# Kernel optimization log

Measured on AMD Instinct MI355X. Metric: run time of the kernel, lower is better.

Reference implementation:

```python
import jax, jax.numpy as jnp
import numpy as np

B, T, F = 2048, 128, 1
H1, H2 = 128, 64


def lstm_relu(x, W, U, b):
    """Keras LSTM with activation=relu, recurrent_activation=sigmoid.
    x: [B, T, Fin]; W: [Fin, 4H]; U: [H, 4H]; b: [4H]. Gate order i,f,g,o.
    Returns full sequence of hidden states [B, T, H]."""
    Bb = x.shape[0]
    H = U.shape[0]

    def step(carry, xt):
        h, c = carry
        z = xt @ W + h @ U + b  # [B, 4H]
        i, f, g, o = jnp.split(z, 4, axis=-1)
        i = jax.nn.sigmoid(i)
        f = jax.nn.sigmoid(f)
        o = jax.nn.sigmoid(o)
        g = jax.nn.relu(g)
        c = f * c + i * g
        h = o * jax.nn.relu(c)
        return (h, c), h

    h0 = jnp.zeros((Bb, H), x.dtype)
    (_, _), hs = jax.lax.scan(step, (h0, h0), jnp.swapaxes(x, 0, 1))
    return jnp.swapaxes(hs, 0, 1)  # [B, T, H]


def setup_inputs() -> dict:
    key = jax.random.key(0)
    ks = jax.random.split(key, 16)
    s = 0.05  # small init so relu LSTM stays numerically stable
    d = {
        "x": jax.random.normal(ks[0], (B, T, F), jnp.float32),
        "W1": jax.random.normal(ks[1], (F, 4 * H1), jnp.float32) * s,
        "U1": jax.random.normal(ks[2], (H1, 4 * H1), jnp.float32) * s,
        "b1": jnp.zeros((4 * H1,), jnp.float32),
        "W2": jax.random.normal(ks[3], (H1, 4 * H2), jnp.float32) * s,
        "U2": jax.random.normal(ks[4], (H2, 4 * H2), jnp.float32) * s,
        "b2": jnp.zeros((4 * H2,), jnp.float32),
        "W3": jax.random.normal(ks[5], (H2, 4 * H2), jnp.float32) * s,
        "U3": jax.random.normal(ks[6], (H2, 4 * H2), jnp.float32) * s,
        "b3": jnp.zeros((4 * H2,), jnp.float32),
        "W4": jax.random.normal(ks[7], (H2, 4 * H1), jnp.float32) * s,
        "U4": jax.random.normal(ks[8], (H1, 4 * H1), jnp.float32) * s,
        "b4": jnp.zeros((4 * H1,), jnp.float32),
        "Wd": jax.random.normal(ks[9], (H1, 1), jnp.float32) * s,
        "bd": jnp.zeros((1,), jnp.float32),
    }
    return d


def reference(x, W1, U1, b1, W2, U2, b2, W3, U3, b3, W4, U4, b4, Wd, bd):
    h = lstm_relu(x, W1, U1, b1)            # [B, T, 128]
    h = lstm_relu(h, W2, U2, b2)[:, -1]     # return_sequences=False -> [B, 64]
    h = jnp.broadcast_to(h[:, None, :], (h.shape[0], T, h.shape[-1]))  # RepeatVector
    h = lstm_relu(h, W3, U3, b3)            # [B, T, 64]
    h = lstm_relu(h, W4, U4, b4)            # [B, T, 128]
    out = h @ Wd + bd                       # TimeDistributed Dense(1) -> [B, T, 1]
    return out
```

## Files before the change

### kernel.cpp

```cpp
#include <hip/hip_runtime.h>


#define TSEQ 128
#define NTH  512
#define BSTR 408

typedef __attribute__((ext_vector_type(8))) short bf16x8;
typedef __attribute__((ext_vector_type(4))) float f32x4;
typedef __attribute__((ext_vector_type(2))) float f32x2;
typedef __attribute__((ext_vector_type(4))) short s16x4;
typedef unsigned short ushort_t;

#define FB_L1 0
#define FB_L2 256
#define FB_L3 448
#define FB_L4 512
#define FB_W3 896
#define WS_FRAGS 960
#define WS_NEEDED (WS_FRAGS * 1024)

__device__ __forceinline__ ushort_t f2bf(float f) {
    union { float f; unsigned u; } a; a.f = f;
    unsigned r = a.u + 0x7FFF + ((a.u >> 16) & 1);
    return (ushort_t)(r >> 16);
}
__device__ __forceinline__ float bf2f(ushort_t h) {
    union { unsigned u; float f; } a; a.u = ((unsigned)h) << 16;
    return a.f;
}
__device__ __forceinline__ float sigm(float z) { return 1.0f / (1.0f + __expf(-z)); }

__device__ __forceinline__ f32x4 MF(bf16x8 a, bf16x8 b, f32x4 c) {
    return __builtin_amdgcn_mfma_f32_16x16x32_bf16(a, b, c, 0, 0, 0);
}

__device__ __forceinline__ unsigned cvtpk(float lo, float hi) {
    unsigned r;
    asm("v_cvt_pk_bf16_f32 %0, %1, %2" : "=v"(r) : "v"(lo), "v"(hi));
    return r;
}

__global__ void pack_weights(const float* __restrict__ U1, const float* __restrict__ W2,
                             const float* __restrict__ U2, const float* __restrict__ U3,
                             const float* __restrict__ W4, const float* __restrict__ U4,
                             const float* __restrict__ W3, ushort_t* __restrict__ out)
{
    const int f = blockIdx.x;
    const int lane = threadIdx.x;
    int fl, KT, ldm, ksplit = 1 << 30, ld2 = 0;
    const float *base, *base2 = nullptr;
    if (f < 256)      { fl = f;       KT = 4; ldm = 512; base = U1; }
    else if (f < 448) { fl = f - 256; KT = 6; ldm = 256; base = W2; ksplit = 128; base2 = U2; ld2 = 256; }
    else if (f < 512) { fl = f - 448; KT = 2; ldm = 256; base = U3; }
    else if (f < 896) { fl = f - 512; KT = 6; ldm = 512; base = W4; ksplit = 64;  base2 = U4; ld2 = 512; }
    else              { fl = f - 896; KT = 2; ldm = 256; base = W3; }
    const int jt = fl / (KT * 2);
    const int rem = fl % (KT * 2);
    const int kt = rem >> 1;
    const int s = rem & 1;
    const int j = jt * 16 + (lane & 15);
    ushort_t* o = out + f * 512 + lane * 8;
    #pragma unroll
    for (int i = 0; i < 8; ++i) {
        const int k = kt * 32 + (lane >> 4) * 8 + i;
        const float w = (k < ksplit) ? base[k * ldm + j] : base2[(k - ksplit) * ld2 + j];
        const ushort_t hi = f2bf(w);
        o[i] = s ? f2bf(w - bf2f(hi)) : hi;
    }
}

__global__ __launch_bounds__(NTH, 1) void lstm_mfma_kernel(
    const float* __restrict__ x,
    const float* __restrict__ W1, const float* __restrict__ b1,
    const float* __restrict__ b2, const float* __restrict__ b3,
    const float* __restrict__ b4,
    const float* __restrict__ Wd, const float* __restrict__ bd,
    const ushort_t* __restrict__ wsp,
    float* __restrict__ out)
{
    __shared__ __align__(16) ushort_t bU[16][BSTR];
    __shared__ __align__(16) float obuf[16][128];
    __shared__ __align__(16) float xls[16][132];
    __shared__ __align__(16) float w1ls[512], b1ls[512], b4ls[512], b2ls[256];
    __shared__ __align__(16) ushort_t wlds[96 * 512];

    const int tid  = threadIdx.x;
    const int wid  = tid >> 6;
    const int lane = tid & 63;
    const int quad = lane >> 4;
    const int l15  = lane & 15;
    const int r0   = blockIdx.x * 16;
    const bf16x8* A = (const bf16x8*)wsp;

    {
        unsigned* p = (unsigned*)&bU[0][0];
        for (int i = tid; i < 16 * BSTR / 2; i += NTH) p[i] = 0u;
        const int srow = tid >> 5, scol = (tid & 31) * 4;
        *(f32x4*)&xls[srow][scol] = *(const f32x4*)&x[(r0 + srow) * TSEQ + scol];
        w1ls[tid] = W1[tid];
        b1ls[tid] = b1[tid];
        b4ls[tid] = b4[tid];
        if (tid < 256) b2ls[tid] = b2[tid];
        const ushort_t* src = wsp + FB_L2 * 512;
        for (int i = tid; i < 96 * 64; i += NTH) {
            const int f = i >> 6, c = (i & 63) * 8;
            *(bf16x8*)&wlds[f * 512 + c] = *(const bf16x8*)&src[f * 1024 + c];
        }
    }

    const int hcb = 16 * wid + quad * 4;
    const float wd0 = Wd[lane], wd1 = Wd[64 + lane], bd0 = bd[0];

    float c1r[4] = {0.f, 0.f, 0.f, 0.f};
    float c4r[4] = {0.f, 0.f, 0.f, 0.f};

    __syncthreads();

    {
        bf16x8 wL1[16];
        #pragma unroll
        for (int q = 0; q < 4; ++q)
            #pragma unroll
            for (int kt = 0; kt < 4; ++kt)
                wL1[q * 4 + kt] = A[(FB_L1 + ((wid + 8 * q) * 4 + kt) * 2) * 64 + lane];
        float c2r[4] = {0.f, 0.f, 0.f, 0.f};

        for (int t = 0; t < TSEQ; ++t) {
            const int rb1 = (t & 1) * 128, wb1 = 128 - rb1;
            const int h2w = 256 + (t & 1) * 64;
            const int h2r = 256 + (((t & 1) ^ 1)) * 64;

            {
                bf16x8 Bh[4];
                #pragma unroll
                for (int kt = 0; kt < 4; ++kt)
                    Bh[kt] = *(const bf16x8*)&bU[l15][rb1 + kt * 32 + quad * 8];
                const float xr = xls[l15][t];
                f32x4 acc[4];
                #pragma unroll
                for (int q = 0; q < 4; ++q) {
                    const int jb = (wid + 8 * q) * 16 + quad * 4;
                    f32x4 a = *(const f32x4*)&b1ls[jb];
                    a += xr * *(const f32x4*)&w1ls[jb];
                    #pragma unroll
                    for (int kt = 0; kt < 4; ++kt)
                        a = MF(wL1[q * 4 + kt], Bh[kt], a);
                    acc[q] = a;
                }
                float hg[4];
                #pragma unroll
                for (int g = 0; g < 4; ++g) {
                    const float zi = acc[0][g];
                    const float zf = acc[1][g];
                    const float zg = acc[2][g];
                    const float zo = acc[3][g];
                    const float c = sigm(zf) * c1r[g] + sigm(zi) * fmaxf(zg, 0.f);
                    c1r[g] = c;
                    hg[g] = sigm(zo) * fmaxf(c, 0.f);
                }
                uint2 hv;
                hv.x = cvtpk(hg[0], hg[1]);
                hv.y = cvtpk(hg[2], hg[3]);
                *(uint2*)&bU[l15][wb1 + hcb] = hv;
            }
            __syncthreads();

            if (wid < 4) {
                bf16x8 Bh[6];
                #pragma unroll
                for (int kt = 0; kt < 4; ++kt)
                    Bh[kt] = *(const bf16x8*)&bU[l15][wb1 + kt * 32 + quad * 8];
                Bh[4] = *(const bf16x8*)&bU[l15][h2r + quad * 8];
                Bh[5] = *(const bf16x8*)&bU[l15][h2r + 32 + quad * 8];
                f32x4 acc[4];
                #pragma unroll
                for (int g = 0; g < 4; ++g) {
                    f32x4 a = *(const f32x4*)&b2ls[(4 * g + wid) * 16 + quad * 4];
                    #pragma unroll
                    for (int kt = 0; kt < 6; ++kt) {
                        const bf16x8 w = *(const bf16x8*)&wlds[((4 * g + wid) * 6 + kt) * 512 + lane * 8];
                        a = MF(w, Bh[kt], a);
                    }
                    acc[g] = a;
                }
                float hg[4];
                #pragma unroll
                for (int e = 0; e < 4; ++e) {
                    const float zi = acc[0][e];
                    const float zf = acc[1][e];
                    const float zg = acc[2][e];
                    const float zo = acc[3][e];
                    const float c = sigm(zf) * c2r[e] + sigm(zi) * fmaxf(zg, 0.f);
                    c2r[e] = c;
                    hg[e] = sigm(zo) * fmaxf(c, 0.f);
                }
                uint2 hv;
                hv.x = cvtpk(hg[0], hg[1]);
                hv.y = cvtpk(hg[2], hg[3]);
                *(uint2*)&bU[l15][h2w + wid * 16 + quad * 4] = hv;
            }
        }
    }
    __syncthreads();

    f32x4 z3r[4];
    if (wid < 4) {
        const bf16x8 Bh0 = *(const bf16x8*)&bU[l15][320 + quad * 8];
        const bf16x8 Bh1 = *(const bf16x8*)&bU[l15][320 + 32 + quad * 8];
        #pragma unroll
        for (int g = 0; g < 4; ++g) {
            const int jt = 4 * g + wid;
            f32x4 a = *(const f32x4*)&b3[jt * 16 + quad * 4];
            a = MF(A[(FB_W3 + (jt * 2 + 0) * 2) * 64 + lane], Bh0, a);
            a = MF(A[(FB_W3 + (jt * 2 + 1) * 2) * 64 + lane], Bh1, a);
            z3r[g] = a;
        }
    }
    __syncthreads();
    {
        unsigned* p = (unsigned*)&bU[0][0];
        for (int i = tid; i < 16 * BSTR / 2; i += NTH) p[i] = 0u;
        c4r[0] = c4r[1] = c4r[2] = c4r[3] = 0.f;
        const ushort_t* src = wsp + FB_L3 * 512;
        for (int i = tid; i < 32 * 64; i += NTH) {
            const int f = i >> 6, c = (i & 63) * 8;
            *(bf16x8*)&wlds[f * 512 + c] = *(const bf16x8*)&src[f * 1024 + c];
        }
    }
    __syncthreads();

    {
        bf16x8 wL4[24];
        #pragma unroll
        for (int q = 0; q < 4; ++q)
            #pragma unroll
            for (int kt = 0; kt < 6; ++kt)
                wL4[q * 6 + kt] = A[(FB_L4 + ((wid + 8 * q) * 6 + kt) * 2) * 64 + lane];
        float c3r[4] = {0.f, 0.f, 0.f, 0.f};

        for (int t = 0; t < TSEQ; ++t) {
            const int rb3 = (t & 1) * 64, wb3 = 64 - rb3;
            const int rb4 = 128 + (t & 1) * 128;
            const int wb4 = (rb4 == 128) ? 256 : 128;

            if (wid < 4) {
                const bf16x8 Bh0 = *(const bf16x8*)&bU[l15][rb3 + quad * 8];
                const bf16x8 Bh1 = *(const bf16x8*)&bU[l15][rb3 + 32 + quad * 8];
                f32x4 acc[4];
                #pragma unroll
                for (int g = 0; g < 4; ++g) {
                    f32x4 a = z3r[g];
                    const bf16x8 w0 = *(const bf16x8*)&wlds[((4 * g + wid) * 2 + 0) * 512 + lane * 8];
                    const bf16x8 w1 = *(const bf16x8*)&wlds[((4 * g + wid) * 2 + 1) * 512 + lane * 8];
                    a = MF(w0, Bh0, a);
                    a = MF(w1, Bh1, a);
                    acc[g] = a;
                }
                float hg[4];
                #pragma unroll
                for (int e = 0; e < 4; ++e) {
                    const float zi = acc[0][e];
                    const float zf = acc[1][e];
                    const float zg = acc[2][e];
                    const float zo = acc[3][e];
                    const float c = sigm(zf) * c3r[e] + sigm(zi) * fmaxf(zg, 0.f);
                    c3r[e] = c;
                    hg[e] = sigm(zo) * fmaxf(c, 0.f);
                }
                uint2 hv;
                hv.x = cvtpk(hg[0], hg[1]);
                hv.y = cvtpk(hg[2], hg[3]);
                *(uint2*)&bU[l15][wb3 + wid * 16 + quad * 4] = hv;
            }
            __syncthreads();

            {
                bf16x8 Bh[6];
                #pragma unroll
                for (int kt = 0; kt < 2; ++kt)
                    Bh[kt] = *(const bf16x8*)&bU[l15][wb3 + kt * 32 + quad * 8];
                #pragma unroll
                for (int kt = 2; kt < 6; ++kt)
                    Bh[kt] = *(const bf16x8*)&bU[l15][rb4 + (kt - 2) * 32 + quad * 8];
                f32x4 acc[4];
                #pragma unroll
                for (int q = 0; q < 4; ++q) {
                    f32x4 a = *(const f32x4*)&b4ls[(wid + 8 * q) * 16 + quad * 4];
                    #pragma unroll
                    for (int kt = 0; kt < 6; ++kt)
                        a = MF(wL4[q * 6 + kt], Bh[kt], a);
                    acc[q] = a;
                }
                float hg[4];
                #pragma unroll
                for (int g = 0; g < 4; ++g) {
                    const float zi = acc[0][g];
                    const float zf = acc[1][g];
                    const float zg = acc[2][g];
                    const float zo = acc[3][g];
                    const float c = sigm(zf) * c4r[g] + sigm(zi) * fmaxf(zg, 0.f);
                    c4r[g] = c;
                    hg[g] = sigm(zo) * fmaxf(c, 0.f);
                }
                uint2 hv;
                hv.x = cvtpk(hg[0], hg[1]);
                hv.y = cvtpk(hg[2], hg[3]);
                *(uint2*)&bU[l15][wb4 + hcb] = hv;
            }

            if (t > 0) {
                #pragma unroll
                for (int e = 0; e < 2; ++e) {
                    const int r = wid + 8 * e;
                    const float h0 = bf2f(bU[r][rb4 + lane]);
                    const float h1_ = bf2f(bU[r][rb4 + 64 + lane]);
                    float v = h0 * wd0 + h1_ * wd1;
                    v += __shfl_down(v, 32);
                    v += __shfl_down(v, 16);
                    v += __shfl_down(v, 8);
                    v += __shfl_down(v, 4);
                    v += __shfl_down(v, 2);
                    v += __shfl_down(v, 1);
                    if (lane == 0) obuf[r][t - 1] = v + bd0;
                }
            }
        }
    }
    __syncthreads();
    {
        #pragma unroll
        for (int e = 0; e < 2; ++e) {
            const int r = wid + 8 * e;
            const float h0 = bf2f(bU[r][128 + lane]);
            const float h1_ = bf2f(bU[r][128 + 64 + lane]);
            float v = h0 * wd0 + h1_ * wd1;
            v += __shfl_down(v, 32);
            v += __shfl_down(v, 16);
            v += __shfl_down(v, 8);
            v += __shfl_down(v, 4);
            v += __shfl_down(v, 2);
            v += __shfl_down(v, 1);
            if (lane == 0) obuf[r][127] = v + bd0;
        }
    }
    __syncthreads();
    {
        const int frow = tid >> 5;
        const int fcol = (tid & 31) * 4;
        *(f32x4*)&out[(r0 + frow) * TSEQ + fcol] = *(const f32x4*)&obuf[frow][fcol];
    }
}

#define FNT 512
#define FRPB 8
__global__ __launch_bounds__(FNT, 2) void lstm_stack_kernel(
    const float* __restrict__ x,
    const float* __restrict__ W1, const float* __restrict__ U1, const float* __restrict__ b1,
    const float* __restrict__ W2, const float* __restrict__ U2, const float* __restrict__ b2,
    const float* __restrict__ W3, const float* __restrict__ U3, const float* __restrict__ b3,
    const float* __restrict__ W4, const float* __restrict__ U4, const float* __restrict__ b4,
    const float* __restrict__ Wd, const float* __restrict__ bd,
    float* __restrict__ out)
{
    __shared__ float h1s[FRPB][128], c1s[FRPB][128];
    __shared__ float h2s[FRPB][64],  c2s[FRPB][64];
    __shared__ float h3s[FRPB][64],  c3s[FRPB][64];
    __shared__ float h4s[FRPB][128], c4s[FRPB][128];
    __shared__ float zbf[FRPB][512];
    __shared__ float z3xf[FRPB][256];
    __shared__ float xs[FRPB];

    const int tid = threadIdx.x;
    const int r0  = blockIdx.x * FRPB;
    const int jg  = tid & 255;
    const int grp = tid >> 8;
    const int rb  = grp * 4;

    {
        float* p1 = &h1s[0][0]; float* p2 = &c1s[0][0];
        float* p3 = &h4s[0][0]; float* p4 = &c4s[0][0];
        for (int i = tid; i < FRPB * 128; i += FNT) { p1[i]=0.f; p2[i]=0.f; p3[i]=0.f; p4[i]=0.f; }
        float* q1 = &h2s[0][0]; float* q2 = &c2s[0][0];
        float* q3 = &h3s[0][0]; float* q4 = &c3s[0][0];
        for (int i = tid; i < FRPB * 64; i += FNT) { q1[i]=0.f; q2[i]=0.f; q3[i]=0.f; q4[i]=0.f; }
    }
    __syncthreads();

    const float w1j = W1[tid];
    const float b1j = b1[tid];
    const float b2j = b2[jg];

    for (int t = 0; t < TSEQ; ++t) {
        if (tid < FRPB) xs[tid] = x[(r0 + tid) * TSEQ + t];
        __syncthreads();
        {
            float acc[FRPB];
            #pragma unroll
            for (int r = 0; r < FRPB; ++r) acc[r] = 0.f;
            const float* Uc = U1 + tid;
            #pragma unroll 4
            for (int k4 = 0; k4 < 32; ++k4) {
                const float u0 = Uc[(k4*4+0)*512];
                const float u1 = Uc[(k4*4+1)*512];
                const float u2 = Uc[(k4*4+2)*512];
                const float u3 = Uc[(k4*4+3)*512];
                #pragma unroll
                for (int r = 0; r < FRPB; ++r) {
                    const float4 h = ((const float4*)h1s[r])[k4];
                    acc[r] += h.x*u0 + h.y*u1 + h.z*u2 + h.w*u3;
                }
            }
            #pragma unroll
            for (int r = 0; r < FRPB; ++r) zbf[r][tid] = acc[r] + xs[r]*w1j + b1j;
        }
        __syncthreads();
        for (int e = tid; e < FRPB * 128; e += FNT) {
            const int r = e >> 7, hc = e & 127;
            const float zi = zbf[r][hc], zf = zbf[r][128+hc], zg = zbf[r][256+hc], zo = zbf[r][384+hc];
            const float c = sigm(zf)*c1s[r][hc] + sigm(zi)*fmaxf(zg, 0.f);
            c1s[r][hc] = c;
            h1s[r][hc] = sigm(zo)*fmaxf(c, 0.f);
        }
        __syncthreads();
        {
            float acc[4] = {0.f, 0.f, 0.f, 0.f};
            const float* Wc = W2 + jg;
            #pragma unroll 4
            for (int k4 = 0; k4 < 32; ++k4) {
                const float u0 = Wc[(k4*4+0)*256];
                const float u1 = Wc[(k4*4+1)*256];
                const float u2 = Wc[(k4*4+2)*256];
                const float u3 = Wc[(k4*4+3)*256];
// ... 84 lines not shown
            c3s[r][hc] = c;
            h3s[r][hc] = sigm(zo)*fmaxf(c, 0.f);
        }
        __syncthreads();
        {
            float acc[FRPB];
            #pragma unroll
            for (int r = 0; r < FRPB; ++r) acc[r] = 0.f;
            const float* Wc = W4 + tid;
            #pragma unroll 4
            for (int k4 = 0; k4 < 16; ++k4) {
                const float u0 = Wc[(k4*4+0)*512];
                const float u1 = Wc[(k4*4+1)*512];
                const float u2 = Wc[(k4*4+2)*512];
                const float u3 = Wc[(k4*4+3)*512];
                #pragma unroll
                for (int r = 0; r < FRPB; ++r) {
                    const float4 h = ((const float4*)h3s[r])[k4];
                    acc[r] += h.x*u0 + h.y*u1 + h.z*u2 + h.w*u3;
                }
            }
            const float* Uc = U4 + tid;
            #pragma unroll 4
            for (int k4 = 0; k4 < 32; ++k4) {
                const float u0 = Uc[(k4*4+0)*512];
                const float u1 = Uc[(k4*4+1)*512];
                const float u2 = Uc[(k4*4+2)*512];
                const float u3 = Uc[(k4*4+3)*512];
                #pragma unroll
                for (int r = 0; r < FRPB; ++r) {
                    const float4 h = ((const float4*)h4s[r])[k4];
                    acc[r] += h.x*u0 + h.y*u1 + h.z*u2 + h.w*u3;
                }
            }
            #pragma unroll
            for (int r = 0; r < FRPB; ++r) zbf[r][tid] = acc[r] + b4j;
        }
        __syncthreads();
        for (int e = tid; e < FRPB * 128; e += FNT) {
            const int r = e >> 7, hc = e & 127;
            const float zi = zbf[r][hc], zf = zbf[r][128+hc], zg = zbf[r][256+hc], zo = zbf[r][384+hc];
            const float c = sigm(zf)*c4s[r][hc] + sigm(zi)*fmaxf(zg, 0.f);
            c4s[r][hc] = c;
            h4s[r][hc] = sigm(zo)*fmaxf(c, 0.f);
        }
        __syncthreads();
        {
            const int wv = tid >> 6, ln = tid & 63;
            float v = h4s[wv][ln]*wd0 + h4s[wv][64+ln]*wd1;
            v += __shfl_down(v, 32, 64);
            v += __shfl_down(v, 16, 64);
            v += __shfl_down(v,  8, 64);
            v += __shfl_down(v,  4, 64);
            v += __shfl_down(v,  2, 64);
            v += __shfl_down(v,  1, 64);
            if (ln == 0) out[(r0 + wv) * TSEQ + t] = v + bd0;
        }
    }
}

extern "C" void kernel_launch(void* const* d_in, const int* in_sizes, int n_in,
                              void* d_out, int out_size, void* d_ws, size_t ws_size,
                              hipStream_t stream) {
    const float* x  = (const float*)d_in[0];
    const float* W1 = (const float*)d_in[1];
    const float* U1 = (const float*)d_in[2];
    const float* b1 = (const float*)d_in[3];
    const float* W2 = (const float*)d_in[4];
    const float* U2 = (const float*)d_in[5];
    const float* b2 = (const float*)d_in[6];
    const float* W3 = (const float*)d_in[7];
    const float* U3 = (const float*)d_in[8];
    const float* b3 = (const float*)d_in[9];
    const float* W4 = (const float*)d_in[10];
    const float* U4 = (const float*)d_in[11];
    const float* b4 = (const float*)d_in[12];
    const float* Wd = (const float*)d_in[13];
    const float* bd = (const float*)d_in[14];
    float* out = (float*)d_out;

    if (ws_size >= (size_t)WS_NEEDED) {
        ushort_t* wsp = (ushort_t*)d_ws;
        pack_weights<<<dim3(WS_FRAGS), dim3(64), 0, stream>>>(U1, W2, U2, U3, W4, U4, W3, wsp);
        lstm_mfma_kernel<<<dim3(2048 / 16), dim3(NTH), 0, stream>>>(
            x, W1, b1, b2, b3, b4, Wd, bd, wsp, out);
    } else {
        lstm_stack_kernel<<<dim3(2048 / FRPB), dim3(FNT), 0, stream>>>(
            x, W1, U1, b1, W2, U2, b2, W3, U3, b3, W4, U4, b4, Wd, bd, out);
    }
}
```

Before: 538.1 us.

## Wavefront-pipeline stacked LSTM layers across warp groups and drop LDS weight cache

Splits the eight waves into two groups that run consecutive LSTM layers concurrently, skewed by one timestep (layer1 on waves 4-7 while layer2 on waves 0-3 processes the previous step; same for layers 3/4), with epilogue steps to drain the pipeline. This leaves one barrier per timestep instead of serialising the two layers. Weights are now streamed from global/L2 each step instead of being held in registers or staged into LDS, and launch bounds are raised to allow two blocks per CU. The trade-off is more global weight traffic per step and half the waves doing layer1/layer4 work, in exchange for overlapping layers and higher occupancy.

```diff
diff --git a/kernel.cpp b/kernel.cpp
--- a/kernel.cpp
+++ b/kernel.cpp
@@ -69,7 +69,7 @@
     }
 }
 
-__global__ __launch_bounds__(NTH, 1) void lstm_mfma_kernel(
+__global__ __launch_bounds__(NTH, 2) void lstm_mfma_kernel(
     const float* __restrict__ x,
     const float* __restrict__ W1, const float* __restrict__ b1,
     const float* __restrict__ b2, const float* __restrict__ b3,
@@ -82,13 +82,13 @@
     __shared__ __align__(16) float obuf[16][128];
     __shared__ __align__(16) float xls[16][132];
     __shared__ __align__(16) float w1ls[512], b1ls[512], b4ls[512], b2ls[256];
-    __shared__ __align__(16) ushort_t wlds[96 * 512];
 
     const int tid  = threadIdx.x;
     const int wid  = tid >> 6;
     const int lane = tid & 63;
     const int quad = lane >> 4;
     const int l15  = lane & 15;
+    const int w4   = wid - 4;
     const int r0   = blockIdx.x * 16;
     const bf16x8* A = (const bf16x8*)wsp;
 
@@ -101,86 +101,74 @@
         b1ls[tid] = b1[tid];
         b4ls[tid] = b4[tid];
         if (tid < 256) b2ls[tid] = b2[tid];
-        const ushort_t* src = wsp + FB_L2 * 512;
-        for (int i = tid; i < 96 * 64; i += NTH) {
-            const int f = i >> 6, c = (i & 63) * 8;
-            *(bf16x8*)&wlds[f * 512 + c] = *(const bf16x8*)&src[f * 1024 + c];
-        }
-    }
-
-    const int hcb = 16 * wid + quad * 4;
+    }
+
     const float wd0 = Wd[lane], wd1 = Wd[64 + lane], bd0 = bd[0];
 
-    float c1r[4] = {0.f, 0.f, 0.f, 0.f};
-    float c4r[4] = {0.f, 0.f, 0.f, 0.f};
-
     __syncthreads();
 
     {
-        bf16x8 wL1[16];
-        #pragma unroll
-        for (int q = 0; q < 4; ++q)
-            #pragma unroll
-            for (int kt = 0; kt < 4; ++kt)
-                wL1[q * 4 + kt] = A[(FB_L1 + ((wid + 8 * q) * 4 + kt) * 2) * 64 + lane];
-        float c2r[4] = {0.f, 0.f, 0.f, 0.f};
+        float c1r[8] = {0.f};
+        float c2r[4] = {0.f};
 
         for (int t = 0; t < TSEQ; ++t) {
+            __syncthreads();
             const int rb1 = (t & 1) * 128, wb1 = 128 - rb1;
-            const int h2w = 256 + (t & 1) * 64;
-            const int h2r = 256 + (((t & 1) ^ 1)) * 64;
-
-            {
+
+            if (wid >= 4) {
                 bf16x8 Bh[4];
                 #pragma unroll
                 for (int kt = 0; kt < 4; ++kt)
                     Bh[kt] = *(const bf16x8*)&bU[l15][rb1 + kt * 32 + quad * 8];
                 const float xr = xls[l15][t];
-                f32x4 acc[4];
-                #pragma unroll
-                for (int q = 0; q < 4; ++q) {
-                    const int jb = (wid + 8 * q) * 16 + quad * 4;
-                    f32x4 a = *(const f32x4*)&b1ls[jb];
-                    a += xr * *(const f32x4*)&w1ls[jb];
+                f32x4 acc[4][2];
+                #pragma unroll
+                for (int g = 0; g < 4; ++g)
                     #pragma unroll
-                    for (int kt = 0; kt < 4; ++kt)
-                        a = MF(wL1[q * 4 + kt], Bh[kt], a);
-                    acc[q] = a;
-                }
-                float hg[4];
-                #pragma unroll
-                for (int g = 0; g < 4; ++g) {
-                    const float zi = acc[0][g];
-                    const float zf = acc[1][g];
-                    const float zg = acc[2][g];
-                    const float zo = acc[3][g];
-                    const float c = sigm(zf) * c1r[g] + sigm(zi) * fmaxf(zg, 0.f);
-                    c1r[g] = c;
-                    hg[g] = sigm(zo) * fmaxf(c, 0.f);
-                }
-                uint2 hv;
-                hv.x = cvtpk(hg[0], hg[1]);
-                hv.y = cvtpk(hg[2], hg[3]);
-                *(uint2*)&bU[l15][wb1 + hcb] = hv;
-            }
-            __syncthreads();
-
-            if (wid < 4) {
+                    for (int d = 0; d < 2; ++d) {
+                        const int jt_ = 8 * g + w4 + 4 * d;
+                        const int jb = jt_ * 16 + quad * 4;
+                        f32x4 a = *(const f32x4*)&b1ls[jb];
+                        a += xr * *(const f32x4*)&w1ls[jb];
+                        #pragma unroll
+                        for (int kt = 0; kt < 4; ++kt)
+                            a = MF(A[(FB_L1 + (jt_ * 4 + kt) * 2) * 64 + lane], Bh[kt], a);
+                        acc[g][d] = a;
+                    }
+                #pragma unroll
+                for (int d = 0; d < 2; ++d) {
+                    float hg[4];
+                    #pragma unroll
+                    for (int g = 0; g < 4; ++g) {
+                        const float zi = acc[0][d][g];
+                        const float zf = acc[1][d][g];
+                        const float zg = acc[2][d][g];
+                        const float zo = acc[3][d][g];
+                        const float c = sigm(zf) * c1r[d * 4 + g] + sigm(zi) * fmaxf(zg, 0.f);
+                        c1r[d * 4 + g] = c;
+                        hg[g] = sigm(zo) * fmaxf(c, 0.f);
+                    }
+                    uint2 hv;
+                    hv.x = cvtpk(hg[0], hg[1]);
+                    hv.y = cvtpk(hg[2], hg[3]);
+                    *(uint2*)&bU[l15][wb1 + (w4 + 4 * d) * 16 + quad * 4] = hv;
+                }
+            } else if (t > 0) {
+                const int h2rd = 256 + (t & 1) * 64;
+                const int h2wr = 256 + ((t & 1) ^ 1) * 64;
                 bf16x8 Bh[6];
                 #pragma unroll
                 for (int kt = 0; kt < 4; ++kt)
-                    Bh[kt] = *(const bf16x8*)&bU[l15][wb1 + kt * 32 + quad * 8];
-                Bh[4] = *(const bf16x8*)&bU[l15][h2r + quad * 8];
-                Bh[5] = *(const bf16x8*)&bU[l15][h2r + 32 + quad * 8];
+                    Bh[kt] = *(const bf16x8*)&bU[l15][rb1 + kt * 32 + quad * 8];
+                Bh[4] = *(const bf16x8*)&bU[l15][h2rd + quad * 8];
+                Bh[5] = *(const bf16x8*)&bU[l15][h2rd + 32 + quad * 8];
                 f32x4 acc[4];
                 #pragma unroll
                 for (int g = 0; g < 4; ++g) {
                     f32x4 a = *(const f32x4*)&b2ls[(4 * g + wid) * 16 + quad * 4];
                     #pragma unroll
-                    for (int kt = 0; kt < 6; ++kt) {
-                        const bf16x8 w = *(const bf16x8*)&wlds[((4 * g + wid) * 6 + kt) * 512 + lane * 8];
-                        a = MF(w, Bh[kt], a);
-                    }
+                    for (int kt = 0; kt < 6; ++kt)
+                        a = MF(A[(FB_L2 + ((4 * g + wid) * 6 + kt) * 2) * 64 + lane], Bh[kt], a);
                     acc[g] = a;
                 }
                 float hg[4];
@@ -197,8 +185,40 @@
                 uint2 hv;
                 hv.x = cvtpk(hg[0], hg[1]);
                 hv.y = cvtpk(hg[2], hg[3]);
-                *(uint2*)&bU[l15][h2w + wid * 16 + quad * 4] = hv;
-            }
+                *(uint2*)&bU[l15][h2wr + wid * 16 + quad * 4] = hv;
+            }
+        }
+        __syncthreads();
+        if (wid < 4) {
+            bf16x8 Bh[6];
+            #pragma unroll
+            for (int kt = 0; kt < 4; ++kt)
+                Bh[kt] = *(const bf16x8*)&bU[l15][0 + kt * 32 + quad * 8];
+            Bh[4] = *(const bf16x8*)&bU[l15][256 + quad * 8];
+            Bh[5] = *(const bf16x8*)&bU[l15][256 + 32 + quad * 8];
+            f32x4 acc[4];
+            #pragma unroll
+            for (int g = 0; g < 4; ++g) {
+                f32x4 a = *(const f32x4*)&b2ls[(4 * g + wid) * 16 + quad * 4];
+                #pragma unroll
+                for (int kt = 0; kt < 6; ++kt)
+                    a = MF(A[(FB_L2 + ((4 * g + wid) * 6 + kt) * 2) * 64 + lane], Bh[kt], a);
+                acc[g] = a;
+            }
+            float hg[4];
+            #pragma unroll
+            for (int e = 0; e < 4; ++e) {
+                const float zi = acc[0][e];
+                const float zf = acc[1][e];
+                const float zg = acc[2][e];
+                const float zo = acc[3][e];
+                const float c = sigm(zf) * c2r[e] + sigm(zi) * fmaxf(zg, 0.f);
+                hg[e] = sigm(zo) * fmaxf(c, 0.f);
+            }
+            uint2 hv;
+            hv.x = cvtpk(hg[0], hg[1]);
+            hv.y = cvtpk(hg[2], hg[3]);
+            *(uint2*)&bU[l15][320 + wid * 16 + quad * 4] = hv;
         }
     }
     __syncthreads();
@@ -220,28 +240,17 @@
     {
         unsigned* p = (unsigned*)&bU[0][0];
         for (int i = tid; i < 16 * BSTR / 2; i += NTH) p[i] = 0u;
-        c4r[0] = c4r[1] = c4r[2] = c4r[3] = 0.f;
-        const ushort_t* src = wsp + FB_L3 * 512;
-        for (int i = tid; i < 32 * 64; i += NTH) {
-            const int f = i >> 6, c = (i & 63) * 8;
-            *(bf16x8*)&wlds[f * 512 + c] = *(const bf16x8*)&src[f * 1024 + c];
-        }
-    }
-    __syncthreads();
+    }
 
     {
-        bf16x8 wL4[24];
-        #pragma unroll
-        for (int q = 0; q < 4; ++q)
-            #pragma unroll
-            for (int kt = 0; kt < 6; ++kt)
-                wL4[q * 6 + kt] = A[(FB_L4 + ((wid + 8 * q) * 6 + kt) * 2) * 64 + lane];
-        float c3r[4] = {0.f, 0.f, 0.f, 0.f};
+        float c3r[4] = {0.f};
+        float c4r[8] = {0.f};
 
         for (int t = 0; t < TSEQ; ++t) {
+            __syncthreads();
             const int rb3 = (t & 1) * 64, wb3 = 64 - rb3;
-            const int rb4 = 128 + (t & 1) * 128;
-            const int wb4 = (rb4 == 128) ? 256 : 128;
+            const int b4rd = 128 + (t & 1) * 128;
+            const int b4wr = 128 + ((t & 1) ^ 1) * 128;
 
             if (wid < 4) {
                 const bf16x8 Bh0 = *(const bf16x8*)&bU[l15][rb3 + quad * 8];
@@ -250,10 +259,8 @@
                 #pragma unroll
                 for (int g = 0; g < 4; ++g) {
                     f32x4 a = z3r[g];
-                    const bf16x8 w0 = *(const bf16x8*)&wlds[((4 * g + wid) * 2 + 0) * 512 + lane * 8];
-                    const bf16x8 w1 = *(const bf16x8*)&wlds[((4 * g + wid) * 2 + 1) * 512 + lane * 8];
-                    a = MF(w0, Bh0, a);
-                    a = MF(w1, Bh1, a);
+                    a = MF(A[(FB_L3 + ((4 * g + wid) * 2 + 0) * 2) * 64 + lane], Bh0, a);
+                    a = MF(A[(FB_L3 + ((4 * g + wid) * 2 + 1) * 2) * 64 + lane], Bh1, a);
                     acc[g] = a;
                 }
                 float hg[4];
@@ -271,76 +278,133 @@
                 hv.x = cvtpk(hg[0], hg[1]);
                 hv.y = cvtpk(hg[2], hg[3]);
                 *(uint2*)&bU[l15][wb3 + wid * 16 + quad * 4] = hv;
-            }
-            __syncthreads();
-
-            {
+
+                if (t > 1) {
+                    #pragma unroll
+                    for (int e = 0; e < 4; ++e) {
+                        const int r = wid + 4 * e;
+                        const float h0 = bf2f(bU[r][b4rd + lane]);
+                        const float h1_ = bf2f(bU[r][b4rd + 64 + lane]);
+                        float v = h0 * wd0 + h1_ * wd1;
+                        v += __shfl_down(v, 32);
+                        v += __shfl_down(v, 16);
+                        v += __shfl_down(v, 8);
+                        v += __shfl_down(v, 4);
+                        v += __shfl_down(v, 2);
+                        v += __shfl_down(v, 1);
+                        if (lane == 0) obuf[r][t - 2] = v + bd0;
+                    }
+                }
+            } else if (t > 0) {
                 bf16x8 Bh[6];
                 #pragma unroll
                 for (int kt = 0; kt < 2; ++kt)
-                    Bh[kt] = *(const bf16x8*)&bU[l15][wb3 + kt * 32 + quad * 8];
+                    Bh[kt] = *(const bf16x8*)&bU[l15][rb3 + kt * 32 + quad * 8];
                 #pragma unroll
                 for (int kt = 2; kt < 6; ++kt)
-                    Bh[kt] = *(const bf16x8*)&bU[l15][rb4 + (kt - 2) * 32 + quad * 8];
-                f32x4 acc[4];
-                #pragma unroll
-                for (int q = 0; q < 4; ++q) {
-                    f32x4 a = *(const f32x4*)&b4ls[(wid + 8 * q) * 16 + quad * 4];
+                    Bh[kt] = *(const bf16x8*)&bU[l15][b4rd + (kt - 2) * 32 + quad * 8];
+                f32x4 acc[4][2];
+                #pragma unroll
+                for (int g = 0; g < 4; ++g)
+                    #pragma unroll
+                    for (int d = 0; d < 2; ++d) {
+                        const int jt_ = 8 * g + w4 + 4 * d;
+                        f32x4 a = *(const f32x4*)&b4ls[jt_ * 16 + quad * 4];
+                        #pragma unroll
+                        for (int kt = 0; kt < 6; ++kt)
+                            a = MF(A[(FB_L4 + (jt_ * 6 + kt) * 2) * 64 + lane], Bh[kt], a);
+                        acc[g][d] = a;
+                    }
+                #pragma unroll
+                for (int d = 0; d < 2; ++d) {
+                    float hg[4];
+                    #pragma unroll
+                    for (int g = 0; g < 4; ++g) {
+                        const float zi = acc[0][d][g];
+                        const float zf = acc[1][d][g];
+                        const float zg = acc[2][d][g];
+                        const float zo = acc[3][d][g];
+                        const float c = sigm(zf) * c4r[d * 4 + g] + sigm(zi) * fmaxf(zg, 0.f);
+                        c4r[d * 4 + g] = c;
+                        hg[g] = sigm(zo) * fmaxf(c, 0.f);
+                    }
+                    uint2 hv;
+                    hv.x = cvtpk(hg[0], hg[1]);
+                    hv.y = cvtpk(hg[2], hg[3]);
+                    *(uint2*)&bU[l15][b4wr + (w4 + 4 * d) * 16 + quad * 4] = hv;
+                }
+            }
+        }
+        __syncthreads();
+        if (wid >= 4) {
+            bf16x8 Bh[6];
+            #pragma unroll
+            for (int kt = 0; kt < 2; ++kt)
+                Bh[kt] = *(const bf16x8*)&bU[l15][0 + kt * 32 + quad * 8];
+            #pragma unroll
+            for (int kt = 2; kt < 6; ++kt)
+                Bh[kt] = *(const bf16x8*)&bU[l15][128 + (kt - 2) * 32 + quad * 8];
+            f32x4 acc[4][2];
+            #pragma unroll
+            for (int g = 0; g < 4; ++g)
+                #pragma unroll
+                for (int d = 0; d < 2; ++d) {
+                    const int jt_ = 8 * g + w4 + 4 * d;
+                    f32x4 a = *(const f32x4*)&b4ls[jt_ * 16 + quad * 4];
                     #pragma unroll
                     for (int kt = 0; kt < 6; ++kt)
-                        a = MF(wL4[q * 6 + kt], Bh[kt], a);
-                    acc[q] = a;
-                }
+                        a = MF(A[(FB_L4 + (jt_ * 6 + kt) * 2) * 64 + lane], Bh[kt], a);
+                    acc[g][d] = a;
+                }
+            #pragma unroll
+            for (int d = 0; d < 2; ++d) {
                 float hg[4];
                 #pragma unroll
                 for (int g = 0; g < 4; ++g) {
-                    const float zi = acc[0][g];
-                    const float zf = acc[1][g];
-                    const float zg = acc[2][g];
-                    const float zo = acc[3][g];
-                    const float c = sigm(zf) * c4r[g] + sigm(zi) * fmaxf(zg, 0.f);
-                    c4r[g] = c;
+                    const float zi = acc[0][d][g];
+                    const float zf = acc[1][d][g];
+                    const float zg = acc[2][d][g];
+                    const float zo = acc[3][d][g];
+                    const float c = sigm(zf) * c4r[d * 4 + g] + sigm(zi) * fmaxf(zg, 0.f);
                     hg[g] = sigm(zo) * fmaxf(c, 0.f);
                 }
                 uint2 hv;
                 hv.x = cvtpk(hg[0], hg[1]);
                 hv.y = cvtpk(hg[2], hg[3]);
-                *(uint2*)&bU[l15][wb4 + hcb] = hv;
-            }
-
-            if (t > 0) {
-                #pragma unroll
-                for (int e = 0; e < 2; ++e) {
-                    const int r = wid + 8 * e;
-                    const float h0 = bf2f(bU[r][rb4 + lane]);
-                    const float h1_ = bf2f(bU[r][rb4 + 64 + lane]);
-                    float v = h0 * wd0 + h1_ * wd1;
-                    v += __shfl_down(v, 32);
-                    v += __shfl_down(v, 16);
-                    v += __shfl_down(v, 8);
-                    v += __shfl_down(v, 4);
-                    v += __shfl_down(v, 2);
-                    v += __shfl_down(v, 1);
-                    if (lane == 0) obuf[r][t - 1] = v + bd0;
-                }
-            }
-        }
-    }
-    __syncthreads();
-    {
-        #pragma unroll
-        for (int e = 0; e < 2; ++e) {
-            const int r = wid + 8 * e;
-            const float h0 = bf2f(bU[r][128 + lane]);
-            const float h1_ = bf2f(bU[r][128 + 64 + lane]);
-            float v = h0 * wd0 + h1_ * wd1;
-            v += __shfl_down(v, 32);
-            v += __shfl_down(v, 16);
-            v += __shfl_down(v, 8);
-            v += __shfl_down(v, 4);
-            v += __shfl_down(v, 2);
-            v += __shfl_down(v, 1);
-            if (lane == 0) obuf[r][127] = v + bd0;
+                *(uint2*)&bU[l15][256 + (w4 + 4 * d) * 16 + quad * 4] = hv;
+            }
+        } else {
+            #pragma unroll
+            for (int e = 0; e < 4; ++e) {
+                const int r = wid + 4 * e;
+                const float h0 = bf2f(bU[r][128 + lane]);
+                const float h1_ = bf2f(bU[r][128 + 64 + lane]);
+                float v = h0 * wd0 + h1_ * wd1;
+                v += __shfl_down(v, 32);
+                v += __shfl_down(v, 16);
+                v += __shfl_down(v, 8);
+                v += __shfl_down(v, 4);
+                v += __shfl_down(v, 2);
+                v += __shfl_down(v, 1);
+                if (lane == 0) obuf[r][126] = v + bd0;
+            }
+        }
+        __syncthreads();
+        if (wid < 4) {
+            #pragma unroll
+            for (int e = 0; e < 4; ++e) {
+                const int r = wid + 4 * e;
+                const float h0 = bf2f(bU[r][256 + lane]);
+                const float h1_ = bf2f(bU[r][256 + 64 + lane]);
+                float v = h0 * wd0 + h1_ * wd1;
+                v += __shfl_down(v, 32);
+                v += __shfl_down(v, 16);
+                v += __shfl_down(v, 8);
+                v += __shfl_down(v, 4);
+                v += __shfl_down(v, 2);
+                v += __shfl_down(v, 1);
+                if (lane == 0) obuf[r][127] = v + bd0;
+            }
         }
     }
     __syncthreads();
```

Measured after the change: 1.353 ms. 2.51x slower.

## Wavefront-pipeline layer pairs across warp groups with one barrier per step

Applied to the files above, without the earlier changes.

The block grows from 8 to 12 waves. Four waves compute layer 2 (and layer 3) while eight waves compute layer 1 (and layer 4) one timestep ahead, so each pair of layers runs as a skewed pipeline with a single barrier per step instead of two. The dense head reduction also moves onto the layer-3 waves and overlaps with layer 4. Weights are no longer staged in LDS or held in registers; they are read from global/L2 on every MFMA, which lowers register and LDS pressure but adds memory traffic inside the recurrent loop.

```diff
diff --git a/kernel.cpp b/kernel.cpp
--- a/kernel.cpp
+++ b/kernel.cpp
@@ -2,7 +2,7 @@
 
 
 #define TSEQ 128
-#define NTH  512
+#define NTH  768
 #define BSTR 408
 
 typedef __attribute__((ext_vector_type(8))) short bf16x8;
@@ -82,55 +82,41 @@
     __shared__ __align__(16) float obuf[16][128];
     __shared__ __align__(16) float xls[16][132];
     __shared__ __align__(16) float w1ls[512], b1ls[512], b4ls[512], b2ls[256];
-    __shared__ __align__(16) ushort_t wlds[96 * 512];
 
     const int tid  = threadIdx.x;
     const int wid  = tid >> 6;
     const int lane = tid & 63;
     const int quad = lane >> 4;
     const int l15  = lane & 15;
+    const int cb   = wid - 4;
     const int r0   = blockIdx.x * 16;
     const bf16x8* A = (const bf16x8*)wsp;
 
     {
         unsigned* p = (unsigned*)&bU[0][0];
         for (int i = tid; i < 16 * BSTR / 2; i += NTH) p[i] = 0u;
-        const int srow = tid >> 5, scol = (tid & 31) * 4;
-        *(f32x4*)&xls[srow][scol] = *(const f32x4*)&x[(r0 + srow) * TSEQ + scol];
-        w1ls[tid] = W1[tid];
-        b1ls[tid] = b1[tid];
-        b4ls[tid] = b4[tid];
+        if (tid < 512) {
+            const int srow = tid >> 5, scol = (tid & 31) * 4;
+            *(f32x4*)&xls[srow][scol] = *(const f32x4*)&x[(r0 + srow) * TSEQ + scol];
+            w1ls[tid] = W1[tid];
+            b1ls[tid] = b1[tid];
+            b4ls[tid] = b4[tid];
+        }
         if (tid < 256) b2ls[tid] = b2[tid];
-        const ushort_t* src = wsp + FB_L2 * 512;
-        for (int i = tid; i < 96 * 64; i += NTH) {
-            const int f = i >> 6, c = (i & 63) * 8;
-            *(bf16x8*)&wlds[f * 512 + c] = *(const bf16x8*)&src[f * 1024 + c];
-        }
-    }
-
-    const int hcb = 16 * wid + quad * 4;
+    }
+
     const float wd0 = Wd[lane], wd1 = Wd[64 + lane], bd0 = bd[0];
 
-    float c1r[4] = {0.f, 0.f, 0.f, 0.f};
-    float c4r[4] = {0.f, 0.f, 0.f, 0.f};
-
     __syncthreads();
 
     {
-        bf16x8 wL1[16];
-        #pragma unroll
-        for (int q = 0; q < 4; ++q)
-            #pragma unroll
-            for (int kt = 0; kt < 4; ++kt)
-                wL1[q * 4 + kt] = A[(FB_L1 + ((wid + 8 * q) * 4 + kt) * 2) * 64 + lane];
+        float c1r[4] = {0.f, 0.f, 0.f, 0.f};
         float c2r[4] = {0.f, 0.f, 0.f, 0.f};
 
-        for (int t = 0; t < TSEQ; ++t) {
+        for (int t = 0; t <= TSEQ; ++t) {
             const int rb1 = (t & 1) * 128, wb1 = 128 - rb1;
-            const int h2w = 256 + (t & 1) * 64;
-            const int h2r = 256 + (((t & 1) ^ 1)) * 64;
-
-            {
+
+            if (t < TSEQ && wid >= 4) {
                 bf16x8 Bh[4];
                 #pragma unroll
                 for (int kt = 0; kt < 4; ++kt)
@@ -138,14 +124,15 @@
                 const float xr = xls[l15][t];
                 f32x4 acc[4];
                 #pragma unroll
-                for (int q = 0; q < 4; ++q) {
-                    const int jb = (wid + 8 * q) * 16 + quad * 4;
+                for (int g = 0; g < 4; ++g) {
+                    const int jt_ = cb + 8 * g;
+                    const int jb = jt_ * 16 + quad * 4;
                     f32x4 a = *(const f32x4*)&b1ls[jb];
                     a += xr * *(const f32x4*)&w1ls[jb];
                     #pragma unroll
                     for (int kt = 0; kt < 4; ++kt)
-                        a = MF(wL1[q * 4 + kt], Bh[kt], a);
-                    acc[q] = a;
+                        a = MF(A[(FB_L1 + (jt_ * 4 + kt) * 2) * 64 + lane], Bh[kt], a);
+                    acc[g] = a;
                 }
                 float hg[4];
                 #pragma unroll
@@ -161,26 +148,23 @@
                 uint2 hv;
                 hv.x = cvtpk(hg[0], hg[1]);
                 hv.y = cvtpk(hg[2], hg[3]);
-                *(uint2*)&bU[l15][wb1 + hcb] = hv;
-            }
-            __syncthreads();
-
-            if (wid < 4) {
+                *(uint2*)&bU[l15][wb1 + cb * 16 + quad * 4] = hv;
+            } else if (t > 0 && wid < 4) {
+                const int h2rd = 256 + (t & 1) * 64;
+                const int h2wr = 256 + ((t & 1) ^ 1) * 64;
                 bf16x8 Bh[6];
                 #pragma unroll
                 for (int kt = 0; kt < 4; ++kt)
-                    Bh[kt] = *(const bf16x8*)&bU[l15][wb1 + kt * 32 + quad * 8];
-                Bh[4] = *(const bf16x8*)&bU[l15][h2r + quad * 8];
-                Bh[5] = *(const bf16x8*)&bU[l15][h2r + 32 + quad * 8];
+                    Bh[kt] = *(const bf16x8*)&bU[l15][rb1 + kt * 32 + quad * 8];
+                Bh[4] = *(const bf16x8*)&bU[l15][h2rd + quad * 8];
+                Bh[5] = *(const bf16x8*)&bU[l15][h2rd + 32 + quad * 8];
                 f32x4 acc[4];
                 #pragma unroll
                 for (int g = 0; g < 4; ++g) {
                     f32x4 a = *(const f32x4*)&b2ls[(4 * g + wid) * 16 + quad * 4];
                     #pragma unroll
-                    for (int kt = 0; kt < 6; ++kt) {
-                        const bf16x8 w = *(const bf16x8*)&wlds[((4 * g + wid) * 6 + kt) * 512 + lane * 8];
-                        a = MF(w, Bh[kt], a);
-                    }
+                    for (int kt = 0; kt < 6; ++kt)
+                        a = MF(A[(FB_L2 + ((4 * g + wid) * 6 + kt) * 2) * 64 + lane], Bh[kt], a);
                     acc[g] = a;
                 }
                 float hg[4];
@@ -197,11 +181,11 @@
                 uint2 hv;
                 hv.x = cvtpk(hg[0], hg[1]);
                 hv.y = cvtpk(hg[2], hg[3]);
-                *(uint2*)&bU[l15][h2w + wid * 16 + quad * 4] = hv;
-            }
-        }
-    }
-    __syncthreads();
+                *(uint2*)&bU[l15][h2wr + wid * 16 + quad * 4] = hv;
+            }
+            __syncthreads();
+        }
+    }
 
     f32x4 z3r[4];
     if (wid < 4) {
@@ -220,76 +204,79 @@
     {
         unsigned* p = (unsigned*)&bU[0][0];
         for (int i = tid; i < 16 * BSTR / 2; i += NTH) p[i] = 0u;
-        c4r[0] = c4r[1] = c4r[2] = c4r[3] = 0.f;
-        const ushort_t* src = wsp + FB_L3 * 512;
-        for (int i = tid; i < 32 * 64; i += NTH) {
-            const int f = i >> 6, c = (i & 63) * 8;
-            *(bf16x8*)&wlds[f * 512 + c] = *(const bf16x8*)&src[f * 1024 + c];
-        }
     }
     __syncthreads();
 
     {
-        bf16x8 wL4[24];
-        #pragma unroll
-        for (int q = 0; q < 4; ++q)
-            #pragma unroll
-            for (int kt = 0; kt < 6; ++kt)
-                wL4[q * 6 + kt] = A[(FB_L4 + ((wid + 8 * q) * 6 + kt) * 2) * 64 + lane];
         float c3r[4] = {0.f, 0.f, 0.f, 0.f};
-
-        for (int t = 0; t < TSEQ; ++t) {
+        float c4r[4] = {0.f, 0.f, 0.f, 0.f};
+
+        for (int t = 0; t <= TSEQ + 1; ++t) {
             const int rb3 = (t & 1) * 64, wb3 = 64 - rb3;
-            const int rb4 = 128 + (t & 1) * 128;
-            const int wb4 = (rb4 == 128) ? 256 : 128;
+            const int b4rd = 128 + (t & 1) * 128;
+            const int b4wr = 128 + ((t & 1) ^ 1) * 128;
 
             if (wid < 4) {
-                const bf16x8 Bh0 = *(const bf16x8*)&bU[l15][rb3 + quad * 8];
-                const bf16x8 Bh1 = *(const bf16x8*)&bU[l15][rb3 + 32 + quad * 8];
+                if (t < TSEQ) {
+                    const bf16x8 Bh0 = *(const bf16x8*)&bU[l15][rb3 + quad * 8];
+                    const bf16x8 Bh1 = *(const bf16x8*)&bU[l15][rb3 + 32 + quad * 8];
+                    f32x4 acc[4];
+                    #pragma unroll
+                    for (int g = 0; g < 4; ++g) {
+                        f32x4 a = z3r[g];
+                        a = MF(A[(FB_L3 + ((4 * g + wid) * 2 + 0) * 2) * 64 + lane], Bh0, a);
+                        a = MF(A[(FB_L3 + ((4 * g + wid) * 2 + 1) * 2) * 64 + lane], Bh1, a);
+                        acc[g] = a;
+                    }
+                    float hg[4];
+                    #pragma unroll
+                    for (int e = 0; e < 4; ++e) {
+                        const float zi = acc[0][e];
+                        const float zf = acc[1][e];
+                        const float zg = acc[2][e];
+                        const float zo = acc[3][e];
+                        const float c = sigm(zf) * c3r[e] + sigm(zi) * fmaxf(zg, 0.f);
+                        c3r[e] = c;
+                        hg[e] = sigm(zo) * fmaxf(c, 0.f);
+                    }
+                    uint2 hv;
+                    hv.x = cvtpk(hg[0], hg[1]);
+                    hv.y = cvtpk(hg[2], hg[3]);
+                    *(uint2*)&bU[l15][wb3 + wid * 16 + quad * 4] = hv;
+                }
+                if (t > 1) {
+                    #pragma unroll
+                    for (int e = 0; e < 4; ++e) {
+                        const int r = wid + 4 * e;
+                        const float h0 = bf2f(bU[r][b4rd + lane]);
+                        const float h1_ = bf2f(bU[r][b4rd + 64 + lane]);
+                        float v = h0 * wd0 + h1_ * wd1;
+                        v += __shfl_down(v, 32);
+                        v += __shfl_down(v, 16);
+                        v += __shfl_down(v, 8);
+                        v += __shfl_down(v, 4);
+                        v += __shfl_down(v, 2);
+                        v += __shfl_down(v, 1);
+                        if (lane == 0) obuf[r][t - 2] = v + bd0;
+                    }
+                }
+            } else if (t > 0 && t <= TSEQ) {
+                bf16x8 Bh[6];
+                #pragma unroll
+                for (int kt = 0; kt < 2; ++kt)
+                    Bh[kt] = *(const bf16x8*)&bU[l15][rb3 + kt * 32 + quad * 8];
+                #pragma unroll
+                for (int kt = 2; kt < 6; ++kt)
+                    Bh[kt] = *(const bf16x8*)&bU[l15][b4rd + (kt - 2) * 32 + quad * 8];
                 f32x4 acc[4];
                 #pragma unroll
                 for (int g = 0; g < 4; ++g) {
-                    f32x4 a = z3r[g];
-                    const bf16x8 w0 = *(const bf16x8*)&wlds[((4 * g + wid) * 2 + 0) * 512 + lane * 8];
-                    const bf16x8 w1 = *(const bf16x8*)&wlds[((4 * g + wid) * 2 + 1) * 512 + lane * 8];
-                    a = MF(w0, Bh0, a);
-                    a = MF(w1, Bh1, a);
-                    acc[g] = a;
-                }
-                float hg[4];
-                #pragma unroll
-                for (int e = 0; e < 4; ++e) {
-                    const float zi = acc[0][e];
-                    const float zf = acc[1][e];
-                    const float zg = acc[2][e];
-                    const float zo = acc[3][e];
-                    const float c = sigm(zf) * c3r[e] + sigm(zi) * fmaxf(zg, 0.f);
-                    c3r[e] = c;
-                    hg[e] = sigm(zo) * fmaxf(c, 0.f);
-                }
-                uint2 hv;
-                hv.x = cvtpk(hg[0], hg[1]);
-                hv.y = cvtpk(hg[2], hg[3]);
-                *(uint2*)&bU[l15][wb3 + wid * 16 + quad * 4] = hv;
-            }
-            __syncthreads();
-
-            {
-                bf16x8 Bh[6];
-                #pragma unroll
-                for (int kt = 0; kt < 2; ++kt)
-                    Bh[kt] = *(const bf16x8*)&bU[l15][wb3 + kt * 32 + quad * 8];
-                #pragma unroll
-                for (int kt = 2; kt < 6; ++kt)
-                    Bh[kt] = *(const bf16x8*)&bU[l15][rb4 + (kt - 2) * 32 + quad * 8];
-                f32x4 acc[4];
-                #pragma unroll
-                for (int q = 0; q < 4; ++q) {
-                    f32x4 a = *(const f32x4*)&b4ls[(wid + 8 * q) * 16 + quad * 4];
+                    const int jt_ = cb + 8 * g;
+                    f32x4 a = *(const f32x4*)&b4ls[jt_ * 16 + quad * 4];
                     #pragma unroll
                     for (int kt = 0; kt < 6; ++kt)
-                        a = MF(wL4[q * 6 + kt], Bh[kt], a);
-                    acc[q] = a;
+                        a = MF(A[(FB_L4 + (jt_ * 6 + kt) * 2) * 64 + lane], Bh[kt], a);
+                    acc[g] = a;
                 }
                 float hg[4];
                 #pragma unroll
@@ -305,46 +292,13 @@
                 uint2 hv;
                 hv.x = cvtpk(hg[0], hg[1]);
                 hv.y = cvtpk(hg[2], hg[3]);
-                *(uint2*)&bU[l15][wb4 + hcb] = hv;
-            }
-
-            if (t > 0) {
-                #pragma unroll
-                for (int e = 0; e < 2; ++e) {
-                    const int r = wid + 8 * e;
-                    const float h0 = bf2f(bU[r][rb4 + lane]);
-                    const float h1_ = bf2f(bU[r][rb4 + 64 + lane]);
-                    float v = h0 * wd0 + h1_ * wd1;
-                    v += __shfl_down(v, 32);
-                    v += __shfl_down(v, 16);
-                    v += __shfl_down(v, 8);
-                    v += __shfl_down(v, 4);
-                    v += __shfl_down(v, 2);
-                    v += __shfl_down(v, 1);
-                    if (lane == 0) obuf[r][t - 1] = v + bd0;
-                }
-            }
-        }
-    }
-    __syncthreads();
-    {
-        #pragma unroll
-        for (int e = 0; e < 2; ++e) {
-            const int r = wid + 8 * e;
-            const float h0 = bf2f(bU[r][128 + lane]);
-            const float h1_ = bf2f(bU[r][128 + 64 + lane]);
-            float v = h0 * wd0 + h1_ * wd1;
-            v += __shfl_down(v, 32);
-            v += __shfl_down(v, 16);
-            v += __shfl_down(v, 8);
-            v += __shfl_down(v, 4);
-            v += __shfl_down(v, 2);
-            v += __shfl_down(v, 1);
-            if (lane == 0) obuf[r][127] = v + bd0;
-        }
-    }
-    __syncthreads();
-    {
+                *(uint2*)&bU[l15][b4wr + cb * 16 + quad * 4] = hv;
+            }
+            __syncthreads();
+        }
+    }
+
+    if (tid < 512) {
         const int frow = tid >> 5;
         const int fcol = (tid & 31) * 4;
         *(f32x4*)&out[(r0 + frow) * TSEQ + fcol] = *(const f32x4*)&obuf[frow][fcol];
```

Measured after the change: 757.7 us. 1.41x slower.

## Shrink rows per block to four and stream weights from global memory

Applied to the files above, without the earlier changes.

Each block now handles 4 batch rows instead of 16, so the grid grows from 128 to 512 blocks and can spread across all CUs, with launch bounds raised to allow several blocks per CU. To make that occupancy possible, the register-resident layer 1 and 4 weights and the LDS copy of layer 2 and 3 weights are removed. Every timestep now fetches weight fragments from global memory instead. The MFMA tiles still span 16 columns, so three quarters of each matrix op is padding, and the sequential recurrence chain per block gains memory latency on every step.

```diff
diff --git a/kernel.cpp b/kernel.cpp
--- a/kernel.cpp
+++ b/kernel.cpp
@@ -3,6 +3,7 @@
 
 #define TSEQ 128
 #define NTH  512
+#define RPB  4
 #define BSTR 408
 
 typedef __attribute__((ext_vector_type(8))) short bf16x8;
@@ -69,7 +70,7 @@
     }
 }
 
-__global__ __launch_bounds__(NTH, 1) void lstm_mfma_kernel(
+__global__ __launch_bounds__(NTH, 4) void lstm_mfma_kernel(
     const float* __restrict__ x,
     const float* __restrict__ W1, const float* __restrict__ b1,
     const float* __restrict__ b2, const float* __restrict__ b3,
@@ -82,30 +83,26 @@
     __shared__ __align__(16) float obuf[16][128];
     __shared__ __align__(16) float xls[16][132];
     __shared__ __align__(16) float w1ls[512], b1ls[512], b4ls[512], b2ls[256];
-    __shared__ __align__(16) ushort_t wlds[96 * 512];
 
     const int tid  = threadIdx.x;
     const int wid  = tid >> 6;
     const int lane = tid & 63;
     const int quad = lane >> 4;
     const int l15  = lane & 15;
-    const int r0   = blockIdx.x * 16;
+    const int r0   = blockIdx.x * RPB;
     const bf16x8* A = (const bf16x8*)wsp;
 
     {
         unsigned* p = (unsigned*)&bU[0][0];
         for (int i = tid; i < 16 * BSTR / 2; i += NTH) p[i] = 0u;
         const int srow = tid >> 5, scol = (tid & 31) * 4;
-        *(f32x4*)&xls[srow][scol] = *(const f32x4*)&x[(r0 + srow) * TSEQ + scol];
+        f32x4 xv = {0.f, 0.f, 0.f, 0.f};
+        if (srow < RPB) xv = *(const f32x4*)&x[(r0 + srow) * TSEQ + scol];
+        *(f32x4*)&xls[srow][scol] = xv;
         w1ls[tid] = W1[tid];
         b1ls[tid] = b1[tid];
         b4ls[tid] = b4[tid];
         if (tid < 256) b2ls[tid] = b2[tid];
-        const ushort_t* src = wsp + FB_L2 * 512;
-        for (int i = tid; i < 96 * 64; i += NTH) {
-            const int f = i >> 6, c = (i & 63) * 8;
-            *(bf16x8*)&wlds[f * 512 + c] = *(const bf16x8*)&src[f * 1024 + c];
-        }
     }
 
     const int hcb = 16 * wid + quad * 4;
@@ -117,12 +114,6 @@
     __syncthreads();
 
     {
-        bf16x8 wL1[16];
-        #pragma unroll
-        for (int q = 0; q < 4; ++q)
-            #pragma unroll
-            for (int kt = 0; kt < 4; ++kt)
-                wL1[q * 4 + kt] = A[(FB_L1 + ((wid + 8 * q) * 4 + kt) * 2) * 64 + lane];
         float c2r[4] = {0.f, 0.f, 0.f, 0.f};
 
         for (int t = 0; t < TSEQ; ++t) {
@@ -144,7 +135,7 @@
                     a += xr * *(const f32x4*)&w1ls[jb];
                     #pragma unroll
                     for (int kt = 0; kt < 4; ++kt)
-                        a = MF(wL1[q * 4 + kt], Bh[kt], a);
+                        a = MF(A[(FB_L1 + ((wid + 8 * q) * 4 + kt) * 2) * 64 + lane], Bh[kt], a);
                     acc[q] = a;
                 }
                 float hg[4];
@@ -177,10 +168,8 @@
                 for (int g = 0; g < 4; ++g) {
                     f32x4 a = *(const f32x4*)&b2ls[(4 * g + wid) * 16 + quad * 4];
                     #pragma unroll
-                    for (int kt = 0; kt < 6; ++kt) {
-                        const bf16x8 w = *(const bf16x8*)&wlds[((4 * g + wid) * 6 + kt) * 512 + lane * 8];
-                        a = MF(w, Bh[kt], a);
-                    }
+                    for (int kt = 0; kt < 6; ++kt)
+                        a = MF(A[(FB_L2 + ((4 * g + wid) * 6 + kt) * 2) * 64 + lane], Bh[kt], a);
                     acc[g] = a;
                 }
                 float hg[4];
@@ -221,21 +210,10 @@
         unsigned* p = (unsigned*)&bU[0][0];
         for (int i = tid; i < 16 * BSTR / 2; i += NTH) p[i] = 0u;
         c4r[0] = c4r[1] = c4r[2] = c4r[3] = 0.f;
-        const ushort_t* src = wsp + FB_L3 * 512;
-        for (int i = tid; i < 32 * 64; i += NTH) {
-            const int f = i >> 6, c = (i & 63) * 8;
-            *(bf16x8*)&wlds[f * 512 + c] = *(const bf16x8*)&src[f * 1024 + c];
-        }
-    }
-    __syncthreads();
-
-    {
-        bf16x8 wL4[24];
-        #pragma unroll
-        for (int q = 0; q < 4; ++q)
-            #pragma unroll
-            for (int kt = 0; kt < 6; ++kt)
-                wL4[q * 6 + kt] = A[(FB_L4 + ((wid + 8 * q) * 6 + kt) * 2) * 64 + lane];
+    }
+    __syncthreads();
+
+    {
         float c3r[4] = {0.f, 0.f, 0.f, 0.f};
 
         for (int t = 0; t < TSEQ; ++t) {
@@ -250,10 +228,8 @@
                 #pragma unroll
                 for (int g = 0; g < 4; ++g) {
                     f32x4 a = z3r[g];
-                    const bf16x8 w0 = *(const bf16x8*)&wlds[((4 * g + wid) * 2 + 0) * 512 + lane * 8];
-                    const bf16x8 w1 = *(const bf16x8*)&wlds[((4 * g + wid) * 2 + 1) * 512 + lane * 8];
-                    a = MF(w0, Bh0, a);
-                    a = MF(w1, Bh1, a);
+                    a = MF(A[(FB_L3 + ((4 * g + wid) * 2 + 0) * 2) * 64 + lane], Bh0, a);
+                    a = MF(A[(FB_L3 + ((4 * g + wid) * 2 + 1) * 2) * 64 + lane], Bh1, a);
                     acc[g] = a;
                 }
                 float hg[4];
@@ -288,7 +264,7 @@
                     f32x4 a = *(const f32x4*)&b4ls[(wid + 8 * q) * 16 + quad * 4];
                     #pragma unroll
                     for (int kt = 0; kt < 6; ++kt)
-                        a = MF(wL4[q * 6 + kt], Bh[kt], a);
+                        a = MF(A[(FB_L4 + ((wid + 8 * q) * 6 + kt) * 2) * 64 + lane], Bh[kt], a);
                     acc[q] = a;
                 }
                 float hg[4];
@@ -312,16 +288,18 @@
                 #pragma unroll
                 for (int e = 0; e < 2; ++e) {
                     const int r = wid + 8 * e;
-                    const float h0 = bf2f(bU[r][rb4 + lane]);
-                    const float h1_ = bf2f(bU[r][rb4 + 64 + lane]);
-                    float v = h0 * wd0 + h1_ * wd1;
-                    v += __shfl_down(v, 32);
-                    v += __shfl_down(v, 16);
-                    v += __shfl_down(v, 8);
-                    v += __shfl_down(v, 4);
-                    v += __shfl_down(v, 2);
-                    v += __shfl_down(v, 1);
-                    if (lane == 0) obuf[r][t - 1] = v + bd0;
+                    if (r < RPB) {
+                        const float h0 = bf2f(bU[r][rb4 + lane]);
+                        const float h1_ = bf2f(bU[r][rb4 + 64 + lane]);
+                        float v = h0 * wd0 + h1_ * wd1;
+                        v += __shfl_down(v, 32);
+                        v += __shfl_down(v, 16);
+                        v += __shfl_down(v, 8);
+                        v += __shfl_down(v, 4);
+                        v += __shfl_down(v, 2);
+                        v += __shfl_down(v, 1);
+                        if (lane == 0) obuf[r][t - 1] = v + bd0;
+                    }
                 }
             }
         }
@@ -331,23 +309,26 @@
         #pragma unroll
         for (int e = 0; e < 2; ++e) {
             const int r = wid + 8 * e;
-            const float h0 = bf2f(bU[r][128 + lane]);
-            const float h1_ = bf2f(bU[r][128 + 64 + lane]);
-            float v = h0 * wd0 + h1_ * wd1;
-            v += __shfl_down(v, 32);
-            v += __shfl_down(v, 16);
-            v += __shfl_down(v, 8);
-            v += __shfl_down(v, 4);
-            v += __shfl_down(v, 2);
-            v += __shfl_down(v, 1);
-            if (lane == 0) obuf[r][127] = v + bd0;
+            if (r < RPB) {
+                const float h0 = bf2f(bU[r][128 + lane]);
+                const float h1_ = bf2f(bU[r][128 + 64 + lane]);
+                float v = h0 * wd0 + h1_ * wd1;
+                v += __shfl_down(v, 32);
+                v += __shfl_down(v, 16);
+                v += __shfl_down(v, 8);
+                v += __shfl_down(v, 4);
+                v += __shfl_down(v, 2);
+                v += __shfl_down(v, 1);
+                if (lane == 0) obuf[r][127] = v + bd0;
+            }
         }
     }
     __syncthreads();
     {
         const int frow = tid >> 5;
         const int fcol = (tid & 31) * 4;
-        *(f32x4*)&out[(r0 + frow) * TSEQ + fcol] = *(const f32x4*)&obuf[frow][fcol];
+        if (frow < RPB)
+            *(f32x4*)&out[(r0 + frow) * TSEQ + fcol] = *(const f32x4*)&obuf[frow][fcol];
     }
 }
 
@@ -598,7 +579,7 @@
     if (ws_size >= (size_t)WS_NEEDED) {
         ushort_t* wsp = (ushort_t*)d_ws;
         pack_weights<<<dim3(WS_FRAGS), dim3(64), 0, stream>>>(U1, W2, U2, U3, W4, U4, W3, wsp);
-        lstm_mfma_kernel<<<dim3(2048 / 16), dim3(NTH), 0, stream>>>(
+        lstm_mfma_kernel<<<dim3(2048 / RPB), dim3(NTH), 0, stream>>>(
             x, W1, b1, b2, b3, b4, Wd, bd, wsp, out);
     } else {
         lstm_stack_kernel<<<dim3(2048 / FRPB), dim3(FNT), 0, stream>>>(
```

Result: slower. 1.814 ms (+237.2%).
